# Performance work log

Measured on AMD Instinct MI355X. Metric: run time of the kernel, lower is better.

Reference implementation:

```python
import jax, jax.numpy as jnp
import numpy as np

BITS = 8
BER = 1e-3
STRIDE = 1
PAD = 1


def _quant_ste(x, bits):
    # symmetric per-tensor fixed-point quantization (Quant in the original repo),
    # straight-through so backward is non-degenerate
    qmax = 2 ** (bits - 1) - 1
    scale = jnp.max(jnp.abs(jax.lax.stop_gradient(x))) / qmax + 1e-12
    q = jnp.clip(jnp.round(x / scale), -(qmax + 1), qmax) * scale
    return x + jax.lax.stop_gradient(q - x)


def _bitflip_fi(x, ber, bits, key):
    # operation_fi / operation_mulfi: quantize to `bits`-bit two's complement and
    # flip (at most) one uniformly chosen bit per element with prob ber*bits.
    qmax = 2 ** (bits - 1) - 1
    scale = jnp.max(jnp.abs(jax.lax.stop_gradient(x))) / qmax + 1e-12
    q = jnp.clip(jnp.round(x / scale), -(qmax + 1), qmax).astype(jnp.int32)
    qt = jnp.bitwise_and(q, 2 ** bits - 1)  # two's complement view
    k1, k2 = jax.random.split(key)
    u = jax.random.uniform(k1, x.shape)
    pos = jax.random.randint(k2, x.shape, 0, bits)
    mask = jnp.where(u < ber * bits, jnp.left_shift(jnp.int32(1), pos), 0)
    qf = jnp.bitwise_xor(qt, mask)
    qs = jnp.where(qf >= 2 ** (bits - 1), qf - 2 ** bits, qf).astype(x.dtype)
    y = qs * scale
    return x + jax.lax.stop_gradient(y - x)


def _unfold(x, kh, kw, pad, stride):
    # torch.nn.functional.unfold: output feature order is (C, kh, kw), C slowest
    B, C, H, W = x.shape
    oh = (H + 2 * pad - kh) // stride + 1
    ow = (W + 2 * pad - kw) // stride + 1
    xp = jnp.pad(x, ((0, 0), (0, 0), (pad, pad), (pad, pad)))
    cols = [xp[:, :, i:i + stride * oh:stride, j:j + stride * ow:stride]
            for i in range(kh) for j in range(kw)]
    unf = jnp.stack(cols, axis=2)  # [B, C, kh*kw, oh, ow]
    return unf.reshape(B, C * kh * kw, oh * ow), oh, ow


def setup_inputs() -> dict:
    key = jax.random.key(0)
    kx, kw = jax.random.split(key)
    x = jax.random.normal(kx, (1, 32, 56, 56), dtype=jnp.float32)
    weight = jax.random.normal(kw, (64, 32, 3, 3), dtype=jnp.float32) * 0.05
    return {"x": x, "weight": weight}


def reference(x, weight):
    key = jax.random.key(42)
    Co, Ci, kh, kw = weight.shape
    wq = _quant_ste(weight, BITS)
    unf, oh, ow = _unfold(x, kh, kw, PAD, STRIDE)      # [B, K, L], K=Ci*kh*kw
    xc = jnp.swapaxes(unf, 1, 2)                        # [B, L, K]
    wf = wq.reshape(Co, -1)                             # [Co, K]
    # broadcast elementwise products of every MAC term (the x1*w1 of the original)
    p = xc[:, None, :, :] * wf[None, :, None, :]        # [B, Co, L, K]
    k1, k2, k3 = jax.random.split(key, 3)
    p = _bitflip_fi(p, BER, BITS, k1)                   # operation_mulfi
    c = jnp.cumsum(p, axis=3)                           # running partial sums
    c_fi = _bitflip_fi(c, BER, BITS, k2)                # operation_fi on partial sums
    y_sum = c_fi[..., -1]
    c_error = (c_fi[..., 1:-1] - c[..., 1:-1]).sum(axis=3)  # injected-error fold-in
    y = y_sum + c_error                                 # [B, Co, L]
    y = _bitflip_fi(y, BER, BITS, k3)                   # operation_fi on outputs
    B = x.shape[0]
    return y.reshape(B, Co, oh, ow)
```

## Files before the change

### kernel.cpp

```cpp
#include <hip/hip_runtime.h>
#include <cstdint>

#define CO   64
#define CI   32
#define HH   56
#define WW   56
#define LL   3136
#define KK   288
#define KH   144
#define NOUT 200704u
#define KG   4
#define TO   32

#define FLIP_LT 34359808u

#define FCAP1 320
#define FCAP2 512

#define CWS_OFF_FLOATS 20480u
#define WS_NEED (81920ull + 4ull * 288ull * 200704ull)

__host__ __device__ inline uint32_t rotl32(uint32_t v, uint32_t r) {
#ifdef __HIP_DEVICE_COMPILE__
  return __builtin_amdgcn_alignbit(v, v, 32u - r);
#else
  return (v << r) | (v >> (32u - r));
#endif
}

__host__ __device__ inline void tf2x32(uint32_t k0, uint32_t k1,
                                       uint32_t x0, uint32_t x1,
                                       uint32_t& o0, uint32_t& o1) {
  uint32_t ks2 = k0 ^ k1 ^ 0x1BD11BDAu;
  uint32_t v0 = x0 + k0, v1 = x1 + k1;
#define TF_R(r) { v0 += v1; v1 = rotl32(v1, r); v1 ^= v0; }
  TF_R(13) TF_R(15) TF_R(26) TF_R(6)
  v0 += k1;  v1 += ks2 + 1u;
  TF_R(17) TF_R(29) TF_R(16) TF_R(24)
  v0 += ks2; v1 += k0 + 2u;
  TF_R(13) TF_R(15) TF_R(26) TF_R(6)
  v0 += k0;  v1 += k1 + 3u;
  TF_R(17) TF_R(29) TF_R(16) TF_R(24)
  v0 += k1;  v1 += ks2 + 4u;
  TF_R(13) TF_R(15) TF_R(26) TF_R(6)
  v0 += ks2; v1 += k0 + 5u;
#undef TF_R
  o0 = v0; o1 = v1;
}

__device__ inline uint32_t rbits(uint32_t k0, uint32_t k1, uint32_t i) {
  uint32_t o0, o1;
  tf2x32(k0, k1, 0u, i, o0, o1);
  return o0 ^ o1;
}

__device__ inline float qround(float xv, float scale, float rs) {
#pragma clang fp contract(off)
  float q0 = xv * rs;
  float er = fmaf(-scale, q0, xv);
  return rintf(fmaf(er, rs, q0));
}

__device__ inline float fi_fwd_skip(float x, float scale,
                                    uint32_t ub, uint32_t kp0, uint32_t kp1,
                                    uint32_t i0) {
#pragma clang fp contract(off)
  float q = rintf(x / scale);
  q = fminf(127.0f, fmaxf(-128.0f, q));
  bool flip = ub < FLIP_LT;
  float y;
  if (__any(flip)) {
    uint32_t pb = rbits(kp0, kp1, i0);
    uint32_t qt = ((uint32_t)(int)q) & 0xFFu;
    uint32_t mask = flip ? (1u << (pb & 7u)) : 0u;
    uint32_t qf = qt ^ mask;
    float qs = (float)(int)(signed char)(qf);
    y = qs * scale;
  } else {
    y = q * scale;
  }
  return x + (y - x);
}

template <int BS>
__device__ inline float block_max(float v) {
  __shared__ float s[BS];
  int t = threadIdx.x;
  __syncthreads();
  s[t] = v; __syncthreads();
  for (int o = BS / 2; o > 0; o >>= 1) {
    if (t < o) s[t] = fmaxf(s[t], s[t + o]);
    __syncthreads();
  }
  return s[0];
}

__global__ __launch_bounds__(256) void k_wmax(const float* __restrict__ w,
                                              unsigned int* __restrict__ mbits) {
  int i = blockIdx.x * 256 + threadIdx.x;
  float m = fabsf(w[i]);
  m = block_max<256>(m);
  if (threadIdx.x == 0) atomicMax(mbits, __float_as_uint(m));
}

__global__ __launch_bounds__(256) void k_wquant(const float* __restrict__ w,
                                                const unsigned int* __restrict__ mbits,
                                                float* __restrict__ wq) {
#pragma clang fp contract(off)
  int i = blockIdx.x * 256 + threadIdx.x;
  float scale = __uint_as_float(*mbits) / 127.0f + 1e-12f;
  float xv = w[i];
  float q = fminf(127.0f, fmaxf(-128.0f, rintf(xv / scale)));
  float y = q * scale;
  wq[i] = xv + (y - xv);
}

__global__ __launch_bounds__(256) void k_maxp(const float* __restrict__ x,
                                              const float* __restrict__ wq,
                                              unsigned int* __restrict__ maxp_bits) {
#pragma clang fp contract(off)
  int k = blockIdx.x;
  int ci = k / 9, r = k % 9, di = r / 3, dj = r % 3;
  const float* xr = x + ci * LL;
  float mx = 0.f;
  for (int l = threadIdx.x; l < LL; l += 256) {
    int oy = l / WW, ox = l % WW;
    int yy = oy + di - 1, xx = ox + dj - 1;
    float v = (yy >= 0 && yy < HH && xx >= 0 && xx < WW) ? xr[yy * WW + xx] : 0.f;
    mx = fmaxf(mx, fabsf(v));
  }
  float mw = 0.f;
  for (int co = threadIdx.x; co < CO; co += 256) mw = fmaxf(mw, fabsf(wq[co * KK + k]));
  mx = block_max<256>(mx);
  mw = block_max<256>(mw);
  if (threadIdx.x == 0) atomicMax(maxp_bits, __float_as_uint(mx * mw));
}

__global__ __launch_bounds__(256) void k_fi1cs(const float* __restrict__ x,
                                               const float* __restrict__ wq,
                                               const unsigned int* __restrict__ scal,
                                               unsigned int* __restrict__ maxc_bits,
                                               float* __restrict__ cws,
                                               uint32_t ku0, uint32_t ku1,
                                               uint32_t kp0, uint32_t kp1) {
#pragma clang fp contract(off)
  __shared__ float sW[KK];
  __shared__ float sP[KH][TO];
  __shared__ uint32_t sCnt;
  __shared__ uint32_t sMeta[FCAP1];
  __shared__ float    sVal[FCAP1];
  int tid = threadIdx.x;
  uint32_t outi0 = blockIdx.x * (uint32_t)TO;
  int co = (int)(outi0 / (uint32_t)LL);
  for (int i = tid; i < KK; i += 256) sW[i] = wq[co * KK + i];
  if (tid == 0) sCnt = 0u;
  __syncthreads();

  int o = tid & 31, s = tid >> 5;
  uint32_t outi = outi0 + (uint32_t)o;
  int l = (int)(outi - (uint32_t)co * LL);
  int oy = l / WW, ox = l % WW;
  float scale_p = __uint_as_float(scal[1]) / 127.0f + 1e-12f;
  float rs_p = 1.0f / scale_p;
  uint32_t ibase = outi * (uint32_t)KK;

  float carry = 0.f, maxc = 0.f;
  for (int half = 0; half < 2; ++half) {
    int kbase = half * KH;
    int k = kbase + s * 18;
    int ci0 = k / 9;
    for (int c2 = 0; c2 < 2; ++c2) {
      const float* xr = x + (ci0 + c2) * LL;
      float xv[9];
      uint32_t ub[9];
#pragma unroll
      for (int di = 0; di < 3; ++di) {
        int yy = oy + di - 1;
        bool yok = (yy >= 0) && (yy < HH);
#pragma unroll
        for (int dj = 0; dj < 3; ++dj) {
          int xx = ox + dj - 1;
          xv[di * 3 + dj] = (yok && xx >= 0 && xx < WW) ? xr[yy * WW + xx] : 0.f;
        }
      }
#pragma unroll
      for (int j = 0; j < 9; ++j)
        ub[j] = rbits(ku0, ku1, ibase + (uint32_t)(k + j));
#pragma unroll
      for (int j = 0; j < 9; ++j) {
        float p = xv[j] * sW[k + j];
        float q = qround(p, scale_p, rs_p);
        float y = q * scale_p;
        sP[k + j - kbase][o] = p + (y - p);
        if (ub[j] < FLIP_LT) {
          uint32_t idx = atomicAdd(&sCnt, 1u);
          if (idx < FCAP1) {
            sMeta[idx] = ((uint32_t)(k + j) << 5) | (uint32_t)o;
            sVal[idx] = p;
          }
        }
      }
      k += 9;
    }
    __syncthreads();
    {
      uint32_t n = sCnt; if (n > FCAP1) n = FCAP1;
      for (uint32_t i2 = (uint32_t)tid; i2 < n; i2 += 256u) {
        uint32_t meta = sMeta[i2];
        float p = sVal[i2];
        uint32_t kg = meta >> 5, oo = meta & 31u;
        uint32_t i0 = (outi0 + oo) * (uint32_t)KK + kg;
        uint32_t pb = rbits(kp0, kp1, i0);
        float q = qround(p, scale_p, rs_p);
        uint32_t qt = ((uint32_t)(int)q) & 0xFFu;
        uint32_t qf = qt ^ (1u << (pb & 7u));
        float qs = (float)(int)(signed char)(qf);
        float yv = qs * scale_p;
        sP[kg - (uint32_t)kbase][oo] = p + (yv - p);
      }
    }
    __syncthreads();
    if (tid < TO) {
      float c = carry;
#pragma unroll 8
      for (int kk = 0; kk < KH; ++kk) {
        c += sP[kk][tid];
        sP[kk][tid] = c;
        maxc = fmaxf(maxc, fabsf(c));
      }
      carry = c;
    }
    if (tid == 255) sCnt = 0u;
    __syncthreads();
    for (int b = s; b < 18; b += 8) {
      int gb = half * 18 + b;
      float4 v0 = {sP[b * 8 + 0][o], sP[b * 8 + 1][o],
                   sP[b * 8 + 2][o], sP[b * 8 + 3][o]};
      float4 v1 = {sP[b * 8 + 4][o], sP[b * 8 + 5][o],
                   sP[b * 8 + 6][o], sP[b * 8 + 7][o]};
      float* op = cws + ((size_t)gb * NOUT + outi) * 8u;
      *(float4*)op = v0;
      *((float4*)op + 1) = v1;
    }
    __syncthreads();
  }
  if (tid < 64) {
#pragma unroll
    for (int off = 32; off > 0; off >>= 1)
      maxc = fmaxf(maxc, __shfl_down(maxc, off));
    if (tid == 0) atomicMax(maxc_bits, __float_as_uint(maxc));
  }
}

template <int J0, bool YS>
__device__ inline void fi2_batch(const float* __restrict__ bp, uint32_t ib, int kb,
                                 float scale_c, float rs_c,
                                 uint32_t ku0, uint32_t ku1, uint32_t lane,
                                 uint32_t* __restrict__ sCnt,
                                 uint32_t* __restrict__ sMeta,
                                 float* __restrict__ sVal,
                                 float& e, float& ys) {
#pragma clang fp contract(off)
  float4 A = *(const float4*)bp;
  float4 B = *(const float4*)(bp + 4);
  float c8[8] = {A.x, A.y, A.z, A.w, B.x, B.y, B.z, B.w};
  uint32_t ub[8];
#pragma unroll
  for (int j = J0; j < 8; ++j) ub[j] = rbits(ku0, ku1, ib + (uint32_t)j);
#pragma unroll
  for (int j = J0; j < 8; ++j) {
    float c = c8[j];
    float q = qround(c, scale_c, rs_c);
    float y = q * scale_c;
    float cf = c + (y - c);
    if (YS && j == 7) ys = cf;
    else             e += (cf - c);
    if (ub[j] < FLIP_LT) {
      uint32_t idx = atomicAdd(sCnt, 1u);
      if (idx < FCAP2) {
        sMeta[idx] = ((uint32_t)(kb + j) << 6) | lane;
        sVal[idx] = c;
      }
    }
  }
}

__global__ __launch_bounds__(256) void k_fi2split(const float* __restrict__ cws,
                                                  const unsigned int* __restrict__ scal,
                                                  unsigned int* __restrict__ maxy_bits,
                                                  float* __restrict__ yout,
                                                  uint32_t ku0, uint32_t ku1,
                                                  uint32_t kp0, uint32_t kp1) {
#pragma clang fp contract(off)
  __shared__ float sE[KG][64];
  __shared__ float sYs[64];
  __shared__ float sEC[64];
  __shared__ float sYsC[64];
  __shared__ uint32_t sCnt;
  __shared__ uint32_t sMeta[FCAP2];
  __shared__ float    sVal[FCAP2];
  int tid = threadIdx.x;
  int lane = tid & 63;
  int kg = tid >> 6;
  if (tid < 64) { sEC[tid] = 0.f; sYsC[tid] = 0.f; }
  if (tid == 0) sCnt = 0u;
  __syncthreads();
  uint32_t outi = blockIdx.x * 64u + (uint32_t)lane;
  float scale_c = __uint_as_float(scal[2]) / 127.0f + 1e-12f;
  float rs_c = 1.0f / scale_c;
  uint32_t ibb = outi * (uint32_t)KK;
  const float* bp0 = cws + (size_t)outi * 8u;
  float e = 0.f, ys = 0.f;
  if (kg == 0) {
    fi2_batch<1, false>(bp0, ibb, 0, scale_c, rs_c, ku0, ku1, (uint32_t)lane,
                        &sCnt, sMeta, sVal, e, ys);
    for (int b = 1; b < 9; ++b)
      fi2_batch<0, false>(bp0 + (size_t)b * NOUT * 8u, ibb + (uint32_t)b * 8u, b * 8,
                          scale_c, rs_c, ku0, ku1, (uint32_t)lane,
                          &sCnt, sMeta, sVal, e, ys);
  } else if (kg == KG - 1) {
    for (int b = 27; b < 35; ++b)
      fi2_batch<0, false>(bp0 + (size_t)b * NOUT * 8u, ibb + (uint32_t)b * 8u, b * 8,
                          scale_c, rs_c, ku0, ku1, (uint32_t)lane,
                          &sCnt, sMeta, sVal, e, ys);
    fi2_batch<0, true>(bp0 + (size_t)35 * NOUT * 8u, ibb + 280u, 280,
                       scale_c, rs_c, ku0, ku1, (uint32_t)lane,
                       &sCnt, sMeta, sVal, e, ys);
  } else {
    int b0 = kg * 9;
    for (int b = b0; b < b0 + 9; ++b)
      fi2_batch<0, false>(bp0 + (size_t)b * NOUT * 8u, ibb + (uint32_t)b * 8u, b * 8,
                          scale_c, rs_c, ku0, ku1, (uint32_t)lane,
                          &sCnt, sMeta, sVal, e, ys);
  }
  sE[kg][lane] = e;
  if (kg == KG - 1) sYs[lane] = ys;
  __syncthreads();
  {
    uint32_t n = sCnt; if (n > FCAP2) n = FCAP2;
    for (uint32_t i2 = (uint32_t)tid; i2 < n; i2 += 256u) {
      uint32_t meta = sMeta[i2];
      float c = sVal[i2];
      uint32_t kx = meta >> 6, ln = meta & 63u;
      uint32_t i0 = (blockIdx.x * 64u + ln) * (uint32_t)KK + kx;
      uint32_t pb = rbits(kp0, kp1, i0);
      float q = qround(c, scale_c, rs_c);
      uint32_t qt = ((uint32_t)(int)q) & 0xFFu;
      uint32_t qf = qt ^ (1u << (pb & 7u));
      float qs = (float)(int)(signed char)(qf);
      float yf = qs * scale_c;
      float cff = c + (yf - c);
      float ysk = q * scale_c;
      float cfs = c + (ysk - c);
      float corr = cff - cfs;
      if (kx == 287u) sYsC[ln] = corr;
      else atomicAdd(&sEC[ln], corr);
    }
  }
  __syncthreads();
  float maxy = 0.f;
  if (tid < 64) {
    float ee = ((sE[0][lane] + sE[1][lane]) + sE[2][lane]) + sE[3][lane];
    float y = (sYs[lane] + sYsC[lane]) + (ee + sEC[lane]);
    yout[outi] = y;
    maxy = fabsf(y);
  }
  maxy = block_max<256>(maxy);
  if (tid == 0) atomicMax(maxy_bits, __float_as_uint(maxy));
}

__global__ __launch_bounds__(64) void k_passC_nostore(const float* __restrict__ x,
                                                      const float* __restrict__ wq,
                                                      const unsigned int* __restrict__ scal,
                                                      unsigned int* __restrict__ maxc_bits,
                                                      uint32_t ku0, uint32_t ku1,
                                                      uint32_t kp0, uint32_t kp1) {
#pragma clang fp contract(off)
  __shared__ float sW[KK];
  int co = blockIdx.y;
  for (int i = threadIdx.x; i < KK; i += 64) sW[i] = wq[co * KK + i];
  __syncthreads();
  int l = blockIdx.x * 64 + threadIdx.x;
  float maxc = 0.f;
  if (l < LL) {
    float scale_p = __uint_as_float(scal[1]) / 127.0f + 1e-12f;
    int oy = l / WW, ox = l % WW;
    uint32_t base = (uint32_t)(co * LL + l) * KK;
    float c = 0.f;
    int k = 0;
    for (int ci = 0; ci < CI; ++ci) {
      const float* xr = x + ci * LL;
#pragma unroll
      for (int di = 0; di < 3; ++di) {
        int yy = oy + di - 1;
        bool yok = (yy >= 0) && (yy < HH);
#pragma unroll
        for (int dj = 0; dj < 3; ++dj, ++k) {
          int xx = ox + dj - 1;
          float xv = (yok && xx >= 0 && xx < WW) ? xr[yy * WW + xx] : 0.f;
          float p = xv * sW[k];
          uint32_t i0 = base + (uint32_t)k;
          uint32_t ub = rbits(ku0, ku1, i0);
          c += fi_fwd_skip(p, scale_p, ub, kp0, kp1, i0);
          maxc = fmaxf(maxc, fabsf(c));
        }
      }
    }
  }
  maxc = block_max<64>(maxc);
  if (threadIdx.x == 0) atomicMax(maxc_bits, __float_as_uint(maxc));
}

__global__ __launch_bounds__(256) void k_passD_rec(const float* __restrict__ x,
                                                   const float* __restrict__ wq,
                                                   const unsigned int* __restrict__ scal,
                                                   unsigned int* __restrict__ maxy_bits,
                                                   float* __restrict__ yout,
                                                   uint32_t ku10, uint32_t ku11,
                                                   uint32_t kp10, uint32_t kp11,
                                                   uint32_t ku20, uint32_t ku21,
                                                   uint32_t kp20, uint32_t kp21) {
#pragma clang fp contract(off)
  __shared__ float sW[KK];
  int co = blockIdx.y;
  for (int i = threadIdx.x; i < KK; i += 256) sW[i] = wq[co * KK + i];
  __syncthreads();
  int l = blockIdx.x * 256 + threadIdx.x;
  float maxy = 0.f;
  if (l < LL) {
    float scale_p = __uint_as_float(scal[1]) / 127.0f + 1e-12f;
    float scale_c = __uint_as_float(scal[2]) / 127.0f + 1e-12f;
    int oy = l / WW, ox = l % WW;
    uint32_t base = (uint32_t)(co * LL + l) * KK;
    float c = 0.f, e = 0.f, ys = 0.f;
    int k = 0;
    for (int ci = 0; ci < CI; ++ci) {
      const float* xr = x + ci * LL;
#pragma unroll
      for (int di = 0; di < 3; ++di) {
        int yy = oy + di - 1;
        bool yok = (yy >= 0) && (yy < HH);
#pragma unroll
        for (int dj = 0; dj < 3; ++dj, ++k) {
          int xx = ox + dj - 1;
          float xv = (yok && xx >= 0 && xx < WW) ? xr[yy * WW + xx] : 0.f;
          float p = xv * sW[k];
          uint32_t i0 = base + (uint32_t)k;
          uint32_t ub1 = rbits(ku10, ku11, i0);
          c += fi_fwd_skip(p, scale_p, ub1, kp10, kp11, i0);
          uint32_t ub2 = rbits(ku20, ku21, i0);
          float cf = fi_fwd_skip(c, scale_c, ub2, kp20, kp21, i0);
          if (k >= 1 && k <= 286) e += (cf - c);
          if (k == 287)           ys = cf;
        }
      }
    }
    float y = ys + e;
    yout[co * LL + l] = y;
    maxy = fabsf(y);
  }
  maxy = block_max<256>(maxy);
  if (threadIdx.x == 0) atomicMax(maxy_bits, __float_as_uint(maxy));
}

__global__ __launch_bounds__(256) void k_passE(float* __restrict__ y,
                                               const unsigned int* __restrict__ scal,
                                               uint32_t ku0, uint32_t ku1,
                                               uint32_t kp0, uint32_t kp1) {
#pragma clang fp contract(off)
  uint32_t i = blockIdx.x * 256u + threadIdx.x;
  float scale_y = __uint_as_float(scal[3]) / 127.0f + 1e-12f;
  uint32_t ub = rbits(ku0, ku1, i);
  y[i] = fi_fwd_skip(y[i], scale_y, ub, kp0, kp1, i);
}

extern "C" void kernel_launch(void* const* d_in, const int* in_sizes, int n_in,
                              void* d_out, int out_size, void* d_ws, size_t ws_size,
                              hipStream_t stream) {
  const float* x = (const float*)d_in[0];
  const float* w = (const float*)d_in[1];
  float* out = (float*)d_out;

  unsigned int* scal = (unsigned int*)d_ws;
  float* wq = (float*)d_ws + 16;
  float* cws = (float*)d_ws + CWS_OFF_FLOATS;
  bool bigws = ws_size >= WS_NEED;

  uint32_t K1[2], K2[2], K3[2];
  tf2x32(0u, 42u, 0u, 0u, K1[0], K1[1]);
  tf2x32(0u, 42u, 0u, 1u, K2[0], K2[1]);
  tf2x32(0u, 42u, 0u, 2u, K3[0], K3[1]);
  auto derive = [](const uint32_t kk[2], uint32_t U[2], uint32_t P[2]) {
    uint32_t kA0, kA1, kB0, kB1, t0, t1;
    tf2x32(kk[0], kk[1], 0u, 0u, kA0, kA1);
    tf2x32(kk[0], kk[1], 0u, 1u, kB0, kB1);
    U[0] = kA0; U[1] = kA1;
    tf2x32(kB0, kB1, 0u, 1u, t0, t1);
    P[0] = t0; P[1] = t1;
  };
  uint32_t U1[2],P1[2],U2[2],P2[2],U3[2],P3[2];
  derive(K1, U1, P1); derive(K2, U2, P2); derive(K3, U3, P3);

  hipMemsetAsync(d_ws, 0, 64, stream);

  k_wmax<<<72, 256, 0, stream>>>(w, scal);
  k_wquant<<<72, 256, 0, stream>>>(w, scal, wq);
  k_maxp<<<KK, 256, 0, stream>>>(x, wq, scal + 1);
  if (bigws) {
    k_fi1cs<<<NOUT / TO, 256, 0, stream>>>(x, wq, scal, scal + 2, cws,
                                           U1[0], U1[1], P1[0], P1[1]);
    k_fi2split<<<3136, 256, 0, stream>>>(cws, scal, scal + 3, out,
                                         U2[0], U2[1], P2[0], P2[1]);
  } else {
    dim3 gC(49, 64);
    k_passC_nostore<<<gC, 64, 0, stream>>>(x, wq, scal, scal + 2,
                                           U1[0], U1[1], P1[0], P1[1]);
    dim3 gR(13, 64);
    k_passD_rec<<<gR, 256, 0, stream>>>(x, wq, scal, scal + 3, out,
                                        U1[0], U1[1], P1[0], P1[1],
                                        U2[0], U2[1], P2[0], P2[1]);
  }
  k_passE<<<NOUT / 256, 256, 0, stream>>>(out, scal,
                                          U3[0], U3[1], P3[0], P3[1]);
}
```

Before: 348.0 us.

## Fuse weight quantization into consumers, prefetch partial-sum batches, wave-gate flip atomics

Drops the separate weight-quantize kernel; each consumer kernel now quantizes weights inline from the per-tensor max. Splits the second fault-injection pass so the next 8-float batch is loaded before the current one is processed, overlapping global loads with the PRNG work. Wraps the shared-memory atomic flip logging in a wave-level any() check so waves with no flip skip that branch entirely. This saves one launch plus its global round trip, in exchange for redundant per-block quantization and higher register pressure from the prefetched batch.

```diff
diff --git a/kernel.cpp b/kernel.cpp
--- a/kernel.cpp
+++ b/kernel.cpp
@@ -61,6 +61,13 @@
   return rintf(fmaf(er, rs, q0));
 }
 
+__device__ inline float wquant(float wv, float scale_w) {
+#pragma clang fp contract(off)
+  float q = fminf(127.0f, fmaxf(-128.0f, rintf(wv / scale_w)));
+  float y = q * scale_w;
+  return wv + (y - wv);
+}
+
 __device__ inline float fi_fwd_skip(float x, float scale,
                                     uint32_t ub, uint32_t kp0, uint32_t kp1,
                                     uint32_t i0) {
@@ -103,25 +110,15 @@
   if (threadIdx.x == 0) atomicMax(mbits, __float_as_uint(m));
 }
 
-__global__ __launch_bounds__(256) void k_wquant(const float* __restrict__ w,
-                                                const unsigned int* __restrict__ mbits,
-                                                float* __restrict__ wq) {
-#pragma clang fp contract(off)
-  int i = blockIdx.x * 256 + threadIdx.x;
-  float scale = __uint_as_float(*mbits) / 127.0f + 1e-12f;
-  float xv = w[i];
-  float q = fminf(127.0f, fmaxf(-128.0f, rintf(xv / scale)));
-  float y = q * scale;
-  wq[i] = xv + (y - xv);
-}
-
 __global__ __launch_bounds__(256) void k_maxp(const float* __restrict__ x,
-                                              const float* __restrict__ wq,
+                                              const float* __restrict__ w,
+                                              const unsigned int* __restrict__ scal,
                                               unsigned int* __restrict__ maxp_bits) {
 #pragma clang fp contract(off)
   int k = blockIdx.x;
   int ci = k / 9, r = k % 9, di = r / 3, dj = r % 3;
   const float* xr = x + ci * LL;
+  float scale_w = __uint_as_float(scal[0]) / 127.0f + 1e-12f;
   float mx = 0.f;
   for (int l = threadIdx.x; l < LL; l += 256) {
     int oy = l / WW, ox = l % WW;
@@ -130,14 +127,15 @@
     mx = fmaxf(mx, fabsf(v));
   }
   float mw = 0.f;
-  for (int co = threadIdx.x; co < CO; co += 256) mw = fmaxf(mw, fabsf(wq[co * KK + k]));
+  for (int co = threadIdx.x; co < CO; co += 256)
+    mw = fmaxf(mw, fabsf(wquant(w[co * KK + k], scale_w)));
   mx = block_max<256>(mx);
   mw = block_max<256>(mw);
   if (threadIdx.x == 0) atomicMax(maxp_bits, __float_as_uint(mx * mw));
 }
 
 __global__ __launch_bounds__(256) void k_fi1cs(const float* __restrict__ x,
-                                               const float* __restrict__ wq,
+                                               const float* __restrict__ w,
                                                const unsigned int* __restrict__ scal,
                                                unsigned int* __restrict__ maxc_bits,
                                                float* __restrict__ cws,
@@ -152,7 +150,8 @@
   int tid = threadIdx.x;
   uint32_t outi0 = blockIdx.x * (uint32_t)TO;
   int co = (int)(outi0 / (uint32_t)LL);
-  for (int i = tid; i < KK; i += 256) sW[i] = wq[co * KK + i];
+  float scale_w = __uint_as_float(scal[0]) / 127.0f + 1e-12f;
+  for (int i = tid; i < KK; i += 256) sW[i] = wquant(w[co * KK + i], scale_w);
   if (tid == 0) sCnt = 0u;
   __syncthreads();
 
@@ -192,11 +191,14 @@
         float q = qround(p, scale_p, rs_p);
         float y = q * scale_p;
         sP[k + j - kbase][o] = p + (y - p);
-        if (ub[j] < FLIP_LT) {
-          uint32_t idx = atomicAdd(&sCnt, 1u);
-          if (idx < FCAP1) {
-            sMeta[idx] = ((uint32_t)(k + j) << 5) | (uint32_t)o;
-            sVal[idx] = p;
+        bool flip = ub[j] < FLIP_LT;
+        if (__any(flip)) {
+          if (flip) {
+            uint32_t idx = atomicAdd(&sCnt, 1u);
+            if (idx < FCAP1) {
+              sMeta[idx] = ((uint32_t)(k + j) << 5) | (uint32_t)o;
+              sVal[idx] = p;
+            }
           }
         }
       }
@@ -253,16 +255,14 @@
 }
 
 template <int J0, bool YS>
-__device__ inline void fi2_batch(const float* __restrict__ bp, uint32_t ib, int kb,
-                                 float scale_c, float rs_c,
-                                 uint32_t ku0, uint32_t ku1, uint32_t lane,
-                                 uint32_t* __restrict__ sCnt,
-                                 uint32_t* __restrict__ sMeta,
-                                 float* __restrict__ sVal,
-                                 float& e, float& ys) {
-#pragma clang fp contract(off)
-  float4 A = *(const float4*)bp;
-  float4 B = *(const float4*)(bp + 4);
+__device__ inline void fi2_core(float4 A, float4 B, uint32_t ib, int kb,
+                                float scale_c, float rs_c,
+                                uint32_t ku0, uint32_t ku1, uint32_t lane,
+                                uint32_t* __restrict__ sCnt,
+                                uint32_t* __restrict__ sMeta,
+                                float* __restrict__ sVal,
+                                float& e, float& ys) {
+#pragma clang fp contract(off)
   float c8[8] = {A.x, A.y, A.z, A.w, B.x, B.y, B.z, B.w};
   uint32_t ub[8];
 #pragma unroll
@@ -275,11 +275,14 @@
     float cf = c + (y - c);
     if (YS && j == 7) ys = cf;
     else             e += (cf - c);
-    if (ub[j] < FLIP_LT) {
-      uint32_t idx = atomicAdd(sCnt, 1u);
-      if (idx < FCAP2) {
-        sMeta[idx] = ((uint32_t)(kb + j) << 6) | lane;
-        sVal[idx] = c;
+    bool flip = ub[j] < FLIP_LT;
+    if (__any(flip)) {
+      if (flip) {
+        uint32_t idx = atomicAdd(sCnt, 1u);
+        if (idx < FCAP2) {
+          sMeta[idx] = ((uint32_t)(kb + j) << 6) | lane;
+          sVal[idx] = c;
+        }
       }
     }
   }
@@ -309,29 +312,57 @@
   float scale_c = __uint_as_float(scal[2]) / 127.0f + 1e-12f;
   float rs_c = 1.0f / scale_c;
   uint32_t ibb = outi * (uint32_t)KK;
-  const float* bp0 = cws + (size_t)outi * 8u;
+  const size_t BSTR = (size_t)NOUT * 8u;
   float e = 0.f, ys = 0.f;
   if (kg == 0) {
-    fi2_batch<1, false>(bp0, ibb, 0, scale_c, rs_c, ku0, ku1, (uint32_t)lane,
-                        &sCnt, sMeta, sVal, e, ys);
-    for (int b = 1; b < 9; ++b)
-      fi2_batch<0, false>(bp0 + (size_t)b * NOUT * 8u, ibb + (uint32_t)b * 8u, b * 8,
-                          scale_c, rs_c, ku0, ku1, (uint32_t)lane,
-                          &sCnt, sMeta, sVal, e, ys);
+    const float* bp = cws + (size_t)outi * 8u;
+    float4 A  = *(const float4*)bp;
+    float4 Bv = *(const float4*)(bp + 4);
+    const float* np = bp + BSTR;
+    float4 An = *(const float4*)np;
+    float4 Bn = *(const float4*)(np + 4);
+    fi2_core<1, false>(A, Bv, ibb, 0, scale_c, rs_c, ku0, ku1, (uint32_t)lane,
+                       &sCnt, sMeta, sVal, e, ys);
+    A = An; Bv = Bn; bp = np;
+    for (int b = 1; b < 9; ++b) {
+      np = bp + BSTR;
+      An = *(const float4*)np;
+      Bn = *(const float4*)(np + 4);
+      fi2_core<0, false>(A, Bv, ibb + (uint32_t)b * 8u, b * 8,
+                         scale_c, rs_c, ku0, ku1, (uint32_t)lane,
+                         &sCnt, sMeta, sVal, e, ys);
+      A = An; Bv = Bn; bp = np;
+    }
   } else if (kg == KG - 1) {
-    for (int b = 27; b < 35; ++b)
-      fi2_batch<0, false>(bp0 + (size_t)b * NOUT * 8u, ibb + (uint32_t)b * 8u, b * 8,
-                          scale_c, rs_c, ku0, ku1, (uint32_t)lane,
-                          &sCnt, sMeta, sVal, e, ys);
-    fi2_batch<0, true>(bp0 + (size_t)35 * NOUT * 8u, ibb + 280u, 280,
-                       scale_c, rs_c, ku0, ku1, (uint32_t)lane,
-                       &sCnt, sMeta, sVal, e, ys);
+    const float* bp = cws + (size_t)outi * 8u + 27u * BSTR;
+    float4 A  = *(const float4*)bp;
+    float4 Bv = *(const float4*)(bp + 4);
+    for (int b = 27; b < 35; ++b) {
+      const float* np = bp + BSTR;
+      float4 An = *(const float4*)np;
+      float4 Bn = *(const float4*)(np + 4);
+      fi2_core<0, false>(A, Bv, ibb + (uint32_t)b * 8u, b * 8,
+                         scale_c, rs_c, ku0, ku1, (uint32_t)lane,
+                         &sCnt, sMeta, sVal, e, ys);
+      A = An; Bv = Bn; bp = np;
+    }
+    fi2_core<0, true>(A, Bv, ibb + 280u, 280,
+                      scale_c, rs_c, ku0, ku1, (uint32_t)lane,
+                      &sCnt, sMeta, sVal, e, ys);
   } else {
     int b0 = kg * 9;
-    for (int b = b0; b < b0 + 9; ++b)
-      fi2_batch<0, false>(bp0 + (size_t)b * NOUT * 8u, ibb + (uint32_t)b * 8u, b * 8,
-                          scale_c, rs_c, ku0, ku1, (uint32_t)lane,
-                          &sCnt, sMeta, sVal, e, ys);
+    const float* bp = cws + (size_t)outi * 8u + (size_t)b0 * BSTR;
+    float4 A  = *(const float4*)bp;
+    float4 Bv = *(const float4*)(bp + 4);
+    for (int b = b0; b < b0 + 9; ++b) {
+      const float* np = bp + BSTR;
+      float4 An = *(const float4*)np;
+      float4 Bn = *(const float4*)(np + 4);
+      fi2_core<0, false>(A, Bv, ibb + (uint32_t)b * 8u, b * 8,
+                         scale_c, rs_c, ku0, ku1, (uint32_t)lane,
+                         &sCnt, sMeta, sVal, e, ys);
+      A = An; Bv = Bn; bp = np;
+    }
   }
   sE[kg][lane] = e;
   if (kg == KG - 1) sYs[lane] = ys;
@@ -370,7 +401,7 @@
 }
 
 __global__ __launch_bounds__(64) void k_passC_nostore(const float* __restrict__ x,
-                                                      const float* __restrict__ wq,
+                                                      const float* __restrict__ w,
                                                       const unsigned int* __restrict__ scal,
                                                       unsigned int* __restrict__ maxc_bits,
                                                       uint32_t ku0, uint32_t ku1,
@@ -378,7 +409,8 @@
 #pragma clang fp contract(off)
   __shared__ float sW[KK];
   int co = blockIdx.y;
-  for (int i = threadIdx.x; i < KK; i += 64) sW[i] = wq[co * KK + i];
+  float scale_w = __uint_as_float(scal[0]) / 127.0f + 1e-12f;
+  for (int i = threadIdx.x; i < KK; i += 64) sW[i] = wquant(w[co * KK + i], scale_w);
   __syncthreads();
   int l = blockIdx.x * 64 + threadIdx.x;
   float maxc = 0.f;
@@ -412,7 +444,7 @@
 }
 
 __global__ __launch_bounds__(256) void k_passD_rec(const float* __restrict__ x,
-                                                   const float* __restrict__ wq,
+                                                   const float* __restrict__ w,
                                                    const unsigned int* __restrict__ scal,
                                                    unsigned int* __restrict__ maxy_bits,
                                                    float* __restrict__ yout,
@@ -423,7 +455,8 @@
 #pragma clang fp contract(off)
   __shared__ float sW[KK];
   int co = blockIdx.y;
-  for (int i = threadIdx.x; i < KK; i += 256) sW[i] = wq[co * KK + i];
+  float scale_w = __uint_as_float(scal[0]) / 127.0f + 1e-12f;
+  for (int i = threadIdx.x; i < KK; i += 256) sW[i] = wquant(w[co * KK + i], scale_w);
   __syncthreads();
   int l = blockIdx.x * 256 + threadIdx.x;
   float maxy = 0.f;
@@ -482,7 +515,6 @@
   float* out = (float*)d_out;
 
   unsigned int* scal = (unsigned int*)d_ws;
-  float* wq = (float*)d_ws + 16;
   float* cws = (float*)d_ws + CWS_OFF_FLOATS;
   bool bigws = ws_size >= WS_NEED;
 
@@ -504,19 +536,18 @@
   hipMemsetAsync(d_ws, 0, 64, stream);
 
   k_wmax<<<72, 256, 0, stream>>>(w, scal);
-  k_wquant<<<72, 256, 0, stream>>>(w, scal, wq);
-  k_maxp<<<KK, 256, 0, stream>>>(x, wq, scal + 1);
+  k_maxp<<<KK, 256, 0, stream>>>(x, w, scal, scal + 1);
   if (bigws) {
-    k_fi1cs<<<NOUT / TO, 256, 0, stream>>>(x, wq, scal, scal + 2, cws,
+    k_fi1cs<<<NOUT / TO, 256, 0, stream>>>(x, w, scal, scal + 2, cws,
                                            U1[0], U1[1], P1[0], P1[1]);
     k_fi2split<<<3136, 256, 0, stream>>>(cws, scal, scal + 3, out,
                                          U2[0], U2[1], P2[0], P2[1]);
   } else {
     dim3 gC(49, 64);
-    k_passC_nostore<<<gC, 64, 0, stream>>>(x, wq, scal, scal + 2,
+    k_passC_nostore<<<gC, 64, 0, stream>>>(x, w, scal, scal + 2,
                                            U1[0], U1[1], P1[0], P1[1]);
     dim3 gR(13, 64);
-    k_passD_rec<<<gR, 256, 0, stream>>>(x, wq, scal, scal + 3, out,
+    k_passD_rec<<<gR, 256, 0, stream>>>(x, w, scal, scal + 3, out,
                                         U1[0], U1[1], P1[0], P1[1],
                                         U2[0], U2[1], P2[0], P2[1]);
   }
```

After: 350.6 us. About the same (+0.7%).
